# Optimization experiments

Hardware: AMD Instinct MI355X
Metric: run time of the kernel (lower is better)

## Reference

```python
import jax, jax.numpy as jnp
import numpy as np

N_NODES = 100000


def gcn_conv(x, src, dst, w, W, b, n):
    # PyG GCNConv with add_self_loops=True, normalize=True.
    loop = jnp.arange(n, dtype=src.dtype)
    s = jnp.concatenate([src, loop])
    d = jnp.concatenate([dst, loop])
    ew = jnp.concatenate([w, jnp.ones((n,), dtype=w.dtype)])
    deg = jax.ops.segment_sum(ew, d, num_segments=n)  # in-degree incl. self loop
    dinv = jnp.where(deg > 0, jax.lax.rsqrt(deg), 0.0)
    norm = dinv[s] * ew * dinv[d]  # [E+N]
    h = x @ W  # [n, out] linear transform (no bias yet)
    msg = h[s] * norm[:, None]  # gather + edge scaling, [E+N, out]
    out = jax.ops.segment_sum(msg, d, num_segments=n)  # scatter-add
    return out + b


def setup_inputs() -> dict:
    key = jax.random.key(0)
    k1, k2, k3, k4, k5, k6, k7 = jax.random.split(key, 7)
    in_dim, hid, out_dim = 256, 128, 128
    E = 1600000
    x = jax.random.normal(k1, (N_NODES, in_dim), dtype=jnp.float32)
    edge_index = jax.random.randint(k2, (2, E), 0, N_NODES, dtype=jnp.int32)
    edge_weight = jax.random.uniform(k3, (E,), dtype=jnp.float32)
    # PyG Linear weight is [out, in]; store transposed [in, out] for x @ W
    W1 = jax.random.normal(k4, (in_dim, hid), dtype=jnp.float32) * (1.0 / np.sqrt(in_dim))
    b1 = jax.random.normal(k5, (hid,), dtype=jnp.float32) * 0.02
    W2 = jax.random.normal(k6, (out_dim, hid), dtype=jnp.float32) * (1.0 / np.sqrt(out_dim))
    b2 = jax.random.normal(k7, (hid,), dtype=jnp.float32) * 0.02
    return {"x": x, "edge_index": edge_index, "edge_weight": edge_weight,
            "W1": W1, "b1": b1, "W2": W2, "b2": b2}


def reference(x, edge_index, edge_weight, W1, b1, W2, b2):
    src, dst = edge_index[0], edge_index[1]
    n = x.shape[0]
    h = gcn_conv(x, src, dst, edge_weight, W1, b1, n)
    h = jax.nn.gelu(h, approximate=False)  # torch.nn.GELU default (erf)
    h = gcn_conv(h, src, dst, edge_weight, W2, b2, n)
    h = jax.nn.gelu(h, approximate=False)
    return h
```

## Files before the change

### kernel.cpp

```cpp
#include <hip/hip_runtime.h>
#include <math.h>


#define HID 128

typedef __attribute__((ext_vector_type(8))) short bf16x8;
typedef __attribute__((ext_vector_type(4))) float f32x4;

__device__ __forceinline__ unsigned short f2bf(float f) {
    unsigned int u = __float_as_uint(f);
    u = (u + 0x7fff + ((u >> 16) & 1)) >> 16;
    return (unsigned short)u;
}
__device__ __forceinline__ float bfu2f(unsigned int lo16) {
    return __uint_as_float(lo16 << 16);
}


__global__ __launch_bounds__(256) void cvt_x_kernel(const float* __restrict__ in,
                                                    unsigned int* __restrict__ outb,
                                                    long total8) {
    long g = (long)blockIdx.x * 256 + threadIdx.x;
    if (g >= total8) return;
    const float4* p = reinterpret_cast<const float4*>(in + g * 8);
    float4 a = p[0], b = p[1];
    uint4 o;
    o.x = (unsigned int)f2bf(a.x) | ((unsigned int)f2bf(a.y) << 16);
    o.y = (unsigned int)f2bf(a.z) | ((unsigned int)f2bf(a.w) << 16);
    o.z = (unsigned int)f2bf(b.x) | ((unsigned int)f2bf(b.y) << 16);
    o.w = (unsigned int)f2bf(b.z) | ((unsigned int)f2bf(b.w) << 16);
    *reinterpret_cast<uint4*>(outb + g * 4) = o;
}

__global__ __launch_bounds__(256) void cvt_wt_kernel(const float* __restrict__ W1,
                                                     unsigned short* __restrict__ Wt1, int K1,
                                                     const float* __restrict__ W2,
                                                     unsigned short* __restrict__ Wt2, int K2) {
    int t = blockIdx.x * 256 + threadIdx.x;
    int n1 = 128 * K1;
    if (t < n1) {
        int k = t % K1, c = t / K1;
        Wt1[c * K1 + k] = f2bf(W1[(size_t)k * 128 + c]);
        return;
    }
    t -= n1;
    if (t < 128 * K2) {
        int k = t % K2, c = t / K2;
        Wt2[c * K2 + k] = f2bf(W2[(size_t)k * 128 + c]);
    }
}


__global__ __launch_bounds__(256) void init_kernel(int* count, int n) {
    int i = blockIdx.x * 256 + threadIdx.x;
    if (i < n) count[i] = 0;
}

__global__ __launch_bounds__(256) void count_kernel(const int* __restrict__ dst,
                                                    int* __restrict__ count,
                                                    int* __restrict__ lpos, int E) {
    int e = blockIdx.x * 256 + threadIdx.x;
    if (e < E) lpos[e] = atomicAdd(&count[dst[e]], 1);
}

__global__ __launch_bounds__(1024) void scan1_kernel(const int* __restrict__ count,
                                                     int* __restrict__ row_start,
                                                     int* __restrict__ partials, int n) {
    __shared__ int sdata[1024];
    int t = threadIdx.x;
    int gid = blockIdx.x * 1024 + t;
    int v = (gid < n) ? count[gid] : 0;
    sdata[t] = v;
    __syncthreads();
    for (int off = 1; off < 1024; off <<= 1) {
        int x = (t >= off) ? sdata[t - off] : 0;
        __syncthreads();
        sdata[t] += x;
        __syncthreads();
    }
    if (gid < n) row_start[gid] = sdata[t] - v;
    if (t == 1023) partials[blockIdx.x] = sdata[t];
}

__global__ __launch_bounds__(1024) void scan2_kernel(int* partials, int nparts) {
    __shared__ int sdata[1024];
    int t = threadIdx.x;
    int v = (t < nparts) ? partials[t] : 0;
    sdata[t] = v;
    __syncthreads();
    for (int off = 1; off < 1024; off <<= 1) {
        int x = (t >= off) ? sdata[t - off] : 0;
        __syncthreads();
        sdata[t] += x;
        __syncthreads();
    }
    if (t < nparts) partials[t] = sdata[t] - v;
}

__global__ __launch_bounds__(256) void finalize_kernel(const int* __restrict__ partials,
                                                       int* __restrict__ row_start,
                                                       int n, int E) {
    int i = blockIdx.x * 256 + threadIdx.x;
    if (i < n) row_start[i] += partials[i >> 10];
    if (i == 0) row_start[n] = E;
}

__global__ __launch_bounds__(256) void fill_kernel(const int* __restrict__ src,
                                                   const int* __restrict__ dst,
                                                   const float* __restrict__ w,
                                                   const int* __restrict__ row_start,
                                                   const int* __restrict__ lpos,
                                                   uint2* __restrict__ csr_sw, int E) {
    int e = blockIdx.x * 256 + threadIdx.x;
    if (e >= E) return;
    int d = dst[e];
    int pos = row_start[d] + lpos[e];
    csr_sw[pos] = make_uint2((unsigned int)src[e], __float_as_uint(w[e]));
}

__global__ __launch_bounds__(256) void dinv_kernel(const uint2* __restrict__ csr_sw,
                                                   const int* __restrict__ row_start,
                                                   float* __restrict__ dinv, int n) {
    int i = blockIdx.x * 256 + threadIdx.x;
    if (i >= n) return;
    float dsum = 1.0f;
    int e1 = row_start[i + 1];
    for (int e = row_start[i]; e < e1; e++) dsum += __uint_as_float(csr_sw[e].y);
    dinv[i] = rsqrtf(dsum);
}

template <int K>
__global__ __launch_bounds__(256) void gemm_mfma_kernel(
        const unsigned short* __restrict__ Ab,
        const unsigned short* __restrict__ Wt,
        unsigned short* __restrict__ Hb,
        int n) {
    __shared__ unsigned short Asl[128][40];
    __shared__ unsigned short Btl[128][40];
    const int t = threadIdx.x;
    const int w = t >> 6;
    const int l = t & 63;
    const int lr = l & 15;
    const int ks = l >> 4;
    const int brow = blockIdx.x * 128;

    f32x4 acc[2][8];
#pragma unroll
    for (int m = 0; m < 2; m++)
#pragma unroll
        for (int j = 0; j < 8; j++) acc[m][j] = (f32x4)(0.f);

    for (int k0 = 0; k0 < K; k0 += 32) {
#pragma unroll
        for (int i = 0; i < 2; i++) {
            int idx = i * 256 + t;
            int r = idx >> 2;
            int c8 = idx & 3;
            int gr = brow + r;
            uint4 v = make_uint4(0u, 0u, 0u, 0u);
            if (gr < n) v = *reinterpret_cast<const uint4*>(&Ab[(size_t)gr * K + k0 + c8 * 8]);
            *reinterpret_cast<uint4*>(&Asl[r][c8 * 8]) = v;
        }
#pragma unroll
        for (int i = 0; i < 2; i++) {
            int idx = i * 256 + t;
            int r = idx >> 2;
            int c8 = idx & 3;
            uint4 v = *reinterpret_cast<const uint4*>(&Wt[(size_t)r * K + k0 + c8 * 8]);
            *reinterpret_cast<uint4*>(&Btl[r][c8 * 8]) = v;
        }
        __syncthreads();

        bf16x8 af[2];
#pragma unroll
        for (int m = 0; m < 2; m++)
            af[m] = *reinterpret_cast<const bf16x8*>(&Asl[w * 32 + m * 16 + lr][ks * 8]);
#pragma unroll
        for (int j = 0; j < 8; j++) {
            bf16x8 bfr = *reinterpret_cast<const bf16x8*>(&Btl[j * 16 + lr][ks * 8]);
            acc[0][j] = __builtin_amdgcn_mfma_f32_16x16x32_bf16(af[0], bfr, acc[0][j], 0, 0, 0);
            acc[1][j] = __builtin_amdgcn_mfma_f32_16x16x32_bf16(af[1], bfr, acc[1][j], 0, 0, 0);
        }
        __syncthreads();
    }

#pragma unroll
    for (int m = 0; m < 2; m++) {
#pragma unroll
        for (int r = 0; r < 4; r++) {
            int row = brow + w * 32 + m * 16 + ks * 4 + r;
            if (row < n) {
#pragma unroll
                for (int j = 0; j < 8; j++)
                    Hb[(size_t)row * 128 + j * 16 + lr] = f2bf(acc[m][j][r]);
            }
        }
    }
}

template <bool BF16_OUT>
__global__ __launch_bounds__(256) void aggregate_gelu_kernel(
        const unsigned int* __restrict__ hb,
        const int* __restrict__ row_start,
        const uint2* __restrict__ csr_sw,
        const float* __restrict__ dinv,
        const float* __restrict__ bias,
        unsigned int* __restrict__ outb,
        float* __restrict__ outf, int n) {
    int node = blockIdx.x * 4 + (threadIdx.x >> 6);
    int c2 = threadIdx.x & 63;
    if (node >= n) return;

    float di = dinv[node];
    float dd = di * di;
    float2 b2 = *reinterpret_cast<const float2*>(&bias[c2 * 2]);
    unsigned int self = hb[(size_t)node * 64 + c2];
    float s0 = 0.f, s1 = 0.f;

    int e = row_start[node];
    const int e1 = row_start[node + 1];

    for (; e + 4 <= e1; e += 4) {
        uint2 ew0 = csr_sw[e],     ew1 = csr_sw[e + 1];
        uint2 ew2 = csr_sw[e + 2], ew3 = csr_sw[e + 3];
        float m0 = __uint_as_float(ew0.y) * dinv[ew0.x];
        float m1 = __uint_as_float(ew1.y) * dinv[ew1.x];
        float m2 = __uint_as_float(ew2.y) * dinv[ew2.x];
        float m3 = __uint_as_float(ew3.y) * dinv[ew3.x];
        unsigned int v0 = hb[(size_t)ew0.x * 64 + c2];
        unsigned int v1 = hb[(size_t)ew1.x * 64 + c2];
        unsigned int v2 = hb[(size_t)ew2.x * 64 + c2];
        unsigned int v3 = hb[(size_t)ew3.x * 64 + c2];
        s0 += m0 * bfu2f(v0 & 0xffffu);  s1 += m0 * bfu2f(v0 >> 16);
        s0 += m1 * bfu2f(v1 & 0xffffu);  s1 += m1 * bfu2f(v1 >> 16);
        s0 += m2 * bfu2f(v2 & 0xffffu);  s1 += m2 * bfu2f(v2 >> 16);
        s0 += m3 * bfu2f(v3 & 0xffffu);  s1 += m3 * bfu2f(v3 >> 16);
    }
    for (; e < e1; e++) {
        uint2 ew = csr_sw[e];
        float m = __uint_as_float(ew.y) * dinv[ew.x];
        unsigned int v = hb[(size_t)ew.x * 64 + c2];
        s0 += m * bfu2f(v & 0xffffu);
        s1 += m * bfu2f(v >> 16);
    }

    float acc0 = b2.x + dd * bfu2f(self & 0xffffu) + di * s0;
    float acc1 = b2.y + dd * bfu2f(self >> 16) + di * s1;
    float g0 = 0.5f * acc0 * (1.0f + erff(acc0 * 0.70710678118654752f));
    float g1 = 0.5f * acc1 * (1.0f + erff(acc1 * 0.70710678118654752f));
    if (BF16_OUT) {
        outb[(size_t)node * 64 + c2] =
            (unsigned int)f2bf(g0) | ((unsigned int)f2bf(g1) << 16);
    } else {
        *reinterpret_cast<float2*>(&outf[(size_t)node * 128 + c2 * 2]) = make_float2(g0, g1);
    }
}


extern "C" void kernel_launch(void* const* d_in, const int* in_sizes, int n_in,
                              void* d_out, int out_size, void* d_ws, size_t ws_size,
                              hipStream_t stream) {
    const float* x  = (const float*)d_in[0];
    const int*   ei = (const int*)d_in[1];
    const float* ew = (const float*)d_in[2];
    const float* W1 = (const float*)d_in[3];
    const float* b1 = (const float*)d_in[4];
    const float* W2 = (const float*)d_in[5];
    const float* b2 = (const float*)d_in[6];

    const int IN = 256;
    const int n = in_sizes[0] / IN;
    const int E = in_sizes[2];
    const int* src = ei;
    const int* dst = ei + E;

    char* wsb = (char*)d_ws;
    size_t off = 0;
    auto alloc = [&](size_t bytes) -> void* {
        void* p = wsb + off;
        off = (off + bytes + 255) & ~(size_t)255;
        return p;
    };
    int*   count     = (int*)alloc((size_t)n * 4);
    int*   lpos      = (int*)alloc((size_t)E * 4);
    int*   row_start = (int*)alloc((size_t)(n + 1) * 4);
    int*   partials  = (int*)alloc(4096);
    float* dinv      = (float*)alloc((size_t)n * 4);
    uint2* csr_sw    = (uint2*)alloc((size_t)E * 8);
    unsigned short* hb  = (unsigned short*)alloc((size_t)n * HID * 2);
    unsigned short* wt1 = (unsigned short*)alloc((size_t)128 * IN * 2);
    unsigned short* wt2 = (unsigned short*)alloc((size_t)128 * HID * 2);

    unsigned short* xb    = (unsigned short*)d_out;
    unsigned short* act1b = (unsigned short*)d_out;
    float* out = (float*)d_out;

    const int nscan = (n + 1023) / 1024;

    long total8 = (long)n * IN / 8;
    hipLaunchKernelGGL(cvt_x_kernel, dim3((unsigned)((total8 + 255) / 256)), dim3(256), 0,
                       stream, x, (unsigned int*)xb, total8);
    int wtot = 128 * IN + 128 * HID;
    hipLaunchKernelGGL(cvt_wt_kernel, dim3((wtot + 255) / 256), dim3(256), 0, stream,
                       W1, wt1, IN, W2, wt2, HID);

    hipLaunchKernelGGL(init_kernel, dim3((n + 255) / 256), dim3(256), 0, stream, count, n);
    hipLaunchKernelGGL(count_kernel, dim3((E + 255) / 256), dim3(256), 0, stream,
                       dst, count, lpos, E);
    hipLaunchKernelGGL(scan1_kernel, dim3(nscan), dim3(1024), 0, stream,
                       count, row_start, partials, n);
    hipLaunchKernelGGL(scan2_kernel, dim3(1), dim3(1024), 0, stream, partials, nscan);
    hipLaunchKernelGGL(finalize_kernel, dim3((n + 255) / 256), dim3(256), 0, stream,
                       partials, row_start, n, E);
    hipLaunchKernelGGL(fill_kernel, dim3((E + 255) / 256), dim3(256), 0, stream,
                       src, dst, ew, row_start, lpos, csr_sw, E);
    hipLaunchKernelGGL(dinv_kernel, dim3((n + 255) / 256), dim3(256), 0, stream,
                       csr_sw, row_start, dinv, n);

    hipLaunchKernelGGL((gemm_mfma_kernel<256>), dim3((n + 127) / 128), dim3(256), 0, stream,
                       xb, wt1, hb, n);
    hipLaunchKernelGGL((aggregate_gelu_kernel<true>), dim3((n + 3) / 4), dim3(256), 0, stream,
                       (const unsigned int*)hb, row_start, csr_sw, dinv, b1,
                       (unsigned int*)act1b, nullptr, n);
    hipLaunchKernelGGL((gemm_mfma_kernel<128>), dim3((n + 127) / 128), dim3(256), 0, stream,
                       act1b, wt2, hb, n);
    hipLaunchKernelGGL((aggregate_gelu_kernel<false>), dim3((n + 3) / 4), dim3(256), 0, stream,
                       (const unsigned int*)hb, row_start, csr_sw, dinv, b2,
                       nullptr, out, n);
}
```

Before: 496.2 us.

## Fuse x conversion with edge counting and prescale CSR weights by source dinv

Merges the fp32-to-bf16 conversion of x into the edge-count kernel so both run in one launch. Adds a pass that multiplies each CSR edge weight by the source node's dinv once, so both aggregation layers no longer gather dinv per edge. The aggregation loop is widened to 8 edges per step to keep more gathers in flight. The cost is an extra read-modify-write pass over the CSR array and higher register use in the aggregation kernel.

Result: faster. 472.6 us (-4.8%).

```diff
diff --git a/kernel.cpp b/kernel.cpp
--- a/kernel.cpp
+++ b/kernel.cpp
@@ -16,20 +16,27 @@
     return __uint_as_float(lo16 << 16);
 }
 
-
-__global__ __launch_bounds__(256) void cvt_x_kernel(const float* __restrict__ in,
-                                                    unsigned int* __restrict__ outb,
-                                                    long total8) {
+__global__ __launch_bounds__(256) void count_cvt_kernel(
+        const int* __restrict__ dst, int* __restrict__ count,
+        int* __restrict__ lpos, int E,
+        const float* __restrict__ x, unsigned int* __restrict__ xb, long total8) {
     long g = (long)blockIdx.x * 256 + threadIdx.x;
-    if (g >= total8) return;
-    const float4* p = reinterpret_cast<const float4*>(in + g * 8);
-    float4 a = p[0], b = p[1];
-    uint4 o;
-    o.x = (unsigned int)f2bf(a.x) | ((unsigned int)f2bf(a.y) << 16);
-    o.y = (unsigned int)f2bf(a.z) | ((unsigned int)f2bf(a.w) << 16);
-    o.z = (unsigned int)f2bf(b.x) | ((unsigned int)f2bf(b.y) << 16);
-    o.w = (unsigned int)f2bf(b.z) | ((unsigned int)f2bf(b.w) << 16);
-    *reinterpret_cast<uint4*>(outb + g * 4) = o;
+    bool docvt = g < total8;
+    float4 a, b;
+    if (docvt) {
+        const float4* p = reinterpret_cast<const float4*>(x + g * 8);
+        a = p[0]; b = p[1];
+    }
+    int e = blockIdx.x * 256 + threadIdx.x;
+    if (e < E) lpos[e] = atomicAdd(&count[dst[e]], 1);
+    if (docvt) {
+        uint4 o;
+        o.x = (unsigned int)f2bf(a.x) | ((unsigned int)f2bf(a.y) << 16);
+        o.y = (unsigned int)f2bf(a.z) | ((unsigned int)f2bf(a.w) << 16);
+        o.z = (unsigned int)f2bf(b.x) | ((unsigned int)f2bf(b.y) << 16);
+        o.w = (unsigned int)f2bf(b.z) | ((unsigned int)f2bf(b.w) << 16);
+        *reinterpret_cast<uint4*>(xb + g * 4) = o;
+    }
 }
 
 __global__ __launch_bounds__(256) void cvt_wt_kernel(const float* __restrict__ W1,
@@ -54,13 +61,6 @@
 __global__ __launch_bounds__(256) void init_kernel(int* count, int n) {
     int i = blockIdx.x * 256 + threadIdx.x;
     if (i < n) count[i] = 0;
-}
-
-__global__ __launch_bounds__(256) void count_kernel(const int* __restrict__ dst,
-                                                    int* __restrict__ count,
-                                                    int* __restrict__ lpos, int E) {
-    int e = blockIdx.x * 256 + threadIdx.x;
-    if (e < E) lpos[e] = atomicAdd(&count[dst[e]], 1);
 }
 
 __global__ __launch_bounds__(1024) void scan1_kernel(const int* __restrict__ count,
@@ -127,6 +127,15 @@
     int e1 = row_start[i + 1];
     for (int e = row_start[i]; e < e1; e++) dsum += __uint_as_float(csr_sw[e].y);
     dinv[i] = rsqrtf(dsum);
+}
+
+__global__ __launch_bounds__(256) void mw_kernel(uint2* __restrict__ csr_sw,
+                                                 const float* __restrict__ dinv, int E) {
+    int e = blockIdx.x * 256 + threadIdx.x;
+    if (e >= E) return;
+    uint2 v = csr_sw[e];
+    v.y = __float_as_uint(__uint_as_float(v.y) * dinv[v.x]);
+    csr_sw[e] = v;
 }
 
 template <int K>
@@ -220,25 +229,38 @@
     int e = row_start[node];
     const int e1 = row_start[node + 1];
 
-    for (; e + 4 <= e1; e += 4) {
-        uint2 ew0 = csr_sw[e],     ew1 = csr_sw[e + 1];
-        uint2 ew2 = csr_sw[e + 2], ew3 = csr_sw[e + 3];
-        float m0 = __uint_as_float(ew0.y) * dinv[ew0.x];
-        float m1 = __uint_as_float(ew1.y) * dinv[ew1.x];
-        float m2 = __uint_as_float(ew2.y) * dinv[ew2.x];
-        float m3 = __uint_as_float(ew3.y) * dinv[ew3.x];
-        unsigned int v0 = hb[(size_t)ew0.x * 64 + c2];
-        unsigned int v1 = hb[(size_t)ew1.x * 64 + c2];
-        unsigned int v2 = hb[(size_t)ew2.x * 64 + c2];
-        unsigned int v3 = hb[(size_t)ew3.x * 64 + c2];
-        s0 += m0 * bfu2f(v0 & 0xffffu);  s1 += m0 * bfu2f(v0 >> 16);
-        s0 += m1 * bfu2f(v1 & 0xffffu);  s1 += m1 * bfu2f(v1 >> 16);
-        s0 += m2 * bfu2f(v2 & 0xffffu);  s1 += m2 * bfu2f(v2 >> 16);
-        s0 += m3 * bfu2f(v3 & 0xffffu);  s1 += m3 * bfu2f(v3 >> 16);
+    for (; e + 8 <= e1; e += 8) {
+        uint2 ew[8];
+#pragma unroll
+        for (int i = 0; i < 8; i++) ew[i] = csr_sw[e + i];
+        unsigned int v[8];
+#pragma unroll
+        for (int i = 0; i < 8; i++) v[i] = hb[(size_t)ew[i].x * 64 + c2];
+#pragma unroll
+        for (int i = 0; i < 8; i++) {
+            float m = __uint_as_float(ew[i].y);
+            s0 += m * bfu2f(v[i] & 0xffffu);
+            s1 += m * bfu2f(v[i] >> 16);
+        }
+    }
+    if (e + 4 <= e1) {
+        uint2 ew[4];
+#pragma unroll
+        for (int i = 0; i < 4; i++) ew[i] = csr_sw[e + i];
+        unsigned int v[4];
+#pragma unroll
+        for (int i = 0; i < 4; i++) v[i] = hb[(size_t)ew[i].x * 64 + c2];
+#pragma unroll
+        for (int i = 0; i < 4; i++) {
+            float m = __uint_as_float(ew[i].y);
+            s0 += m * bfu2f(v[i] & 0xffffu);
+            s1 += m * bfu2f(v[i] >> 16);
+        }
+        e += 4;
     }
     for (; e < e1; e++) {
         uint2 ew = csr_sw[e];
-        float m = __uint_as_float(ew.y) * dinv[ew.x];
+        float m = __uint_as_float(ew.y);
         unsigned int v = hb[(size_t)ew.x * 64 + c2];
         s0 += m * bfu2f(v & 0xffffu);
         s1 += m * bfu2f(v >> 16);
@@ -296,17 +318,15 @@
     float* out = (float*)d_out;
 
     const int nscan = (n + 1023) / 1024;
-
     long total8 = (long)n * IN / 8;
-    hipLaunchKernelGGL(cvt_x_kernel, dim3((unsigned)((total8 + 255) / 256)), dim3(256), 0,
-                       stream, x, (unsigned int*)xb, total8);
-    int wtot = 128 * IN + 128 * HID;
-    hipLaunchKernelGGL(cvt_wt_kernel, dim3((wtot + 255) / 256), dim3(256), 0, stream,
-                       W1, wt1, IN, W2, wt2, HID);
+    int cvtBlocks = (int)((total8 + 255) / 256);
+    int fusedBlocks = cvtBlocks > (E + 255) / 256 ? cvtBlocks : (E + 255) / 256;
 
     hipLaunchKernelGGL(init_kernel, dim3((n + 255) / 256), dim3(256), 0, stream, count, n);
-    hipLaunchKernelGGL(count_kernel, dim3((E + 255) / 256), dim3(256), 0, stream,
-                       dst, count, lpos, E);
+    hipLaunchKernelGGL(count_cvt_kernel, dim3(fusedBlocks), dim3(256), 0, stream,
+                       dst, count, lpos, E, x, (unsigned int*)xb, total8);
+    hipLaunchKernelGGL(cvt_wt_kernel, dim3((128 * IN + 128 * HID + 255) / 256), dim3(256),
+                       0, stream, W1, wt1, IN, W2, wt2, HID);
     hipLaunchKernelGGL(scan1_kernel, dim3(nscan), dim3(1024), 0, stream,
                        count, row_start, partials, n);
     hipLaunchKernelGGL(scan2_kernel, dim3(1), dim3(1024), 0, stream, partials, nscan);
@@ -316,6 +336,8 @@
                        src, dst, ew, row_start, lpos, csr_sw, E);
     hipLaunchKernelGGL(dinv_kernel, dim3((n + 255) / 256), dim3(256), 0, stream,
                        csr_sw, row_start, dinv, n);
+    hipLaunchKernelGGL(mw_kernel, dim3((E + 255) / 256), dim3(256), 0, stream,
+                       csr_sw, dinv, E);
 
     hipLaunchKernelGGL((gemm_mfma_kernel<256>), dim3((n + 127) / 128), dim3(256), 0, stream,
                        xb, wt1, hb, n);
```
